# Kernel tuning notes

Measured on AMD Instinct MI355X. Metric: run time of the kernel, lower is better.

Reference implementation:

```python
import jax, jax.numpy as jnp
import numpy as np


def _lstm_layer(x, w_ih, w_hh, b_ih, b_hh):
    """Single LSTM layer, batch_first x: [B, T, D] -> [B, T, H]. Gate order i,f,g,o."""
    B, T, _ = x.shape
    H = w_hh.shape[1]
    # Precompute input-to-gates for all timesteps: [B, T, 4H]
    xg = jnp.einsum('btd,gd->btg', x, w_ih) + b_ih + b_hh

    def step(carry, xg_t):
        h, c = carry
        g = xg_t + h @ w_hh.T  # [B, 4H]
        i, f, gg, o = jnp.split(g, 4, axis=-1)
        i = jax.nn.sigmoid(i)
        f = jax.nn.sigmoid(f)
        gg = jnp.tanh(gg)
        o = jax.nn.sigmoid(o)
        c = f * c + i * gg
        h = o * jnp.tanh(c)
        return (h, c), h

    h0 = jnp.zeros((B, H), x.dtype)
    (_, _), hs = jax.lax.scan(step, (h0, h0), jnp.swapaxes(xg, 0, 1))
    return jnp.swapaxes(hs, 0, 1)  # [B, T, H]


def setup_inputs() -> dict:
    key = jax.random.key(0)
    ks = jax.random.split(key, 11)
    B, T, E, H = 128, 512, 256, 512
    s_e = 1.0 / np.sqrt(H)
    inp = {
        'x': jax.random.normal(ks[0], (B, T, E), jnp.float32),
        'w_ih0': jax.random.uniform(ks[1], (4 * H, E), jnp.float32, -s_e, s_e),
        'w_hh0': jax.random.uniform(ks[2], (4 * H, H), jnp.float32, -s_e, s_e),
        'b_ih0': jax.random.uniform(ks[3], (4 * H,), jnp.float32, -s_e, s_e),
        'b_hh0': jax.random.uniform(ks[4], (4 * H,), jnp.float32, -s_e, s_e),
        'w_ih1': jax.random.uniform(ks[5], (4 * H, H), jnp.float32, -s_e, s_e),
        'w_hh1': jax.random.uniform(ks[6], (4 * H, H), jnp.float32, -s_e, s_e),
        'b_ih1': jax.random.uniform(ks[7], (4 * H,), jnp.float32, -s_e, s_e),
        'b_hh1': jax.random.uniform(ks[8], (4 * H,), jnp.float32, -s_e, s_e),
        'w_fc': jax.random.uniform(ks[9], (1, H), jnp.float32, -s_e, s_e),
        'b_fc': jax.random.uniform(ks[10], (1,), jnp.float32, -s_e, s_e),
    }
    return inp


def reference(x, w_ih0, w_hh0, b_ih0, b_hh0, w_ih1, w_hh1, b_ih1, b_hh1, w_fc, b_fc):
    h1 = _lstm_layer(x, w_ih0, w_hh0, b_ih0, b_hh0)   # [B, T, H]
    h2 = _lstm_layer(h1, w_ih1, w_hh1, b_ih1, b_hh1)  # [B, T, H]
    last = h2[:, -1, :]                               # [B, H]
    out = last @ w_fc.T + b_fc                        # [B, 1]
    return jax.nn.sigmoid(out)
```

## Files before the change

kernel.cpp:

```cpp
#include <hip/hip_runtime.h>

using u16    = unsigned short;
using u64_t  = unsigned long long;
using short4v = __attribute__((ext_vector_type(4))) short;
using short8 = __attribute__((ext_vector_type(8))) short;
using f32x4  = __attribute__((ext_vector_type(4))) float;

#define T_STEPS 512
#define BATCH   128
#define HDIM    512
#define EDIM    256
#define NWG     256
#define WGS     256
#define HPITCH  65536

__device__ __forceinline__ u16 f2bf(float f) {
  unsigned u = __float_as_uint(f);
  u += 0x7FFFu + ((u >> 16) & 1u);
  return (u16)(u >> 16);
}
__device__ __forceinline__ float bf2f(u16 h) {
  return __uint_as_float(((unsigned)h) << 16);
}
__device__ __forceinline__ float sigm(float x) { return 1.0f / (1.0f + __expf(-x)); }
__device__ __forceinline__ float ftanh(float x) { return 1.0f - 2.0f / (__expf(2.0f * x) + 1.0f); }

__device__ __forceinline__ u64_t cl8(const u16* p) {
  return __hip_atomic_load((const u64_t*)p, __ATOMIC_RELAXED, __HIP_MEMORY_SCOPE_AGENT);
}
__device__ __forceinline__ void cstore2(u16* p, u16 v) {
  __hip_atomic_store(p, v, __ATOMIC_RELAXED, __HIP_MEMORY_SCOPE_AGENT);
}
__device__ __forceinline__ void cstore4(int* p, int v) {
  __hip_atomic_store(p, v, __ATOMIC_RELAXED, __HIP_MEMORY_SCOPE_AGENT);
}
__device__ __forceinline__ int ld4(const int* p) {
  return __hip_atomic_load(p, __ATOMIC_RELAXED, __HIP_MEMORY_SCOPE_AGENT);
}
__device__ __forceinline__ int addag(int* p, int v) {
  return __hip_atomic_fetch_add(p, v, __ATOMIC_RELAXED, __HIP_MEMORY_SCOPE_AGENT);
}
__device__ __forceinline__ short8 mk8(u64_t lo, u64_t hi) {
  short4v a = __builtin_bit_cast(short4v, lo);
  short4v b = __builtin_bit_cast(short4v, hi);
  return __builtin_shufflevector(a, b, 0, 1, 2, 3, 4, 5, 6, 7);
}

__global__ void cvt_bf16_kernel(const float* __restrict__ src, u16* __restrict__ dst, int n4) {
  int i = blockIdx.x * blockDim.x + threadIdx.x;
  if (i >= n4) return;
  float4 v = ((const float4*)src)[i];
  uint2 o;
  o.x = (unsigned)f2bf(v.x) | ((unsigned)f2bf(v.y) << 16);
  o.y = (unsigned)f2bf(v.z) | ((unsigned)f2bf(v.w) << 16);
  ((uint2*)dst)[i] = o;
}


__device__ __forceinline__ void grid_barrier(int* cnt, int* root, int* rel,
                                             int it, int tid, int bid) {
  __syncthreads();
  if (tid == 0) {
    int* mycnt = cnt + (bid >> 5) * 64;
    int old = addag(mycnt, 1);
    if (old == 32 * (it + 1) - 1) {
      int r = addag(root, 1);
      if (r == 8 * (it + 1) - 1) cstore4(rel, it + 1);
    }
    while (ld4(rel) < it + 1) __builtin_amdgcn_s_sleep(1);
  }
  __syncthreads();
}

__global__ void __launch_bounds__(WGS, 1) lstm_kernel(
    const float* __restrict__ wih0, const float* __restrict__ whh0,
    const float* __restrict__ bih0, const float* __restrict__ bhh0,
    const float* __restrict__ wih1, const float* __restrict__ whh1,
    const float* __restrict__ bih1, const float* __restrict__ bhh1,
    const float* __restrict__ wfc,  const float* __restrict__ bfc,
    const u16* __restrict__ xbf, u16* __restrict__ h0buf, u16* __restrict__ h1buf,
    float* __restrict__ out, int* syncp, int hist)
{
  extern __shared__ u16 smem[];
  u16* Ws_in  = smem;
  u16* Ws_rec = smem + 16384;

  const int tid    = threadIdx.x;
  const int bid    = blockIdx.x;
  const int layer  = bid >> 7;
  const int lb     = bid & 127;
  const int mhalf  = lb & 1;
  const int nc     = lb >> 1;
  const int jbase  = nc * 8;
  const int w      = tid >> 6;
  const int lane   = tid & 63;
  const int l15    = lane & 15;
  const int q      = lane >> 4;
  const int wmbase = mhalf * 64 + w * 16;
  const int gid    = layer * 2 + mhalf;

  char* sb = (char*)syncp;

  const int K_in = layer ? HDIM : EDIM;
  const float* Wih = layer ? wih1 : wih0;
  const float* Whh = layer ? whh1 : whh0;
  const float* Bih = layer ? bih1 : bih0;
  const float* Bhh = layer ? bhh1 : bhh0;

  for (int p = tid; p < 32 * (K_in / 8); p += WGS) {
    int c = p >> 5, n = p & 31;
    int grow = (n >> 3) * HDIM + jbase + (n & 7);
    const float* s = Wih + (size_t)grow * K_in + c * 8;
    u16* d = Ws_in + p * 8;
    #pragma unroll
    for (int e = 0; e < 8; ++e) d[e] = f2bf(s[e]);
  }
  for (int p = tid; p < 32 * (HDIM / 8); p += WGS) {
    int c = p >> 5, n = p & 31;
    int grow = (n >> 3) * HDIM + jbase + (n & 7);
    const float* s = Whh + (size_t)grow * HDIM + c * 8;
    u16* d = Ws_rec + p * 8;
    #pragma unroll
    for (int e = 0; e < 8; ++e) d[e] = f2bf(s[e]);
  }

  const int cc = l15 & 7;
  const float bi_i = Bih[0*HDIM + jbase + cc] + Bhh[0*HDIM + jbase + cc];
  const float bi_f = Bih[1*HDIM + jbase + cc] + Bhh[1*HDIM + jbase + cc];
  const float bi_g = Bih[2*HDIM + jbase + cc] + Bhh[2*HDIM + jbase + cc];
  const float bi_o = Bih[3*HDIM + jbase + cc] + Bhh[3*HDIM + jbase + cc];

  __syncthreads();

  float cst[4] = {0.f, 0.f, 0.f, 0.f};
  u16* ownbuf = layer ? h1buf : h0buf;
  const int arow = wmbase + l15;
  const size_t cbase = ((size_t)q * 128 + arow) * 8;

  auto MM2 = [&](short8 a, const u16* Ws, int kk, f32x4& A0, f32x4& A1) {
    const u16* bb = Ws + (kk * 4 + q) * 256 + l15 * 8;
    short8 b0 = *(const short8*)bb;
    short8 b1 = *(const short8*)(bb + 128);
    A0 = __builtin_amdgcn_mfma_f32_16x16x32_bf16(a, b0, A0, 0, 0, 0);
    A1 = __builtin_amdgcn_mfma_f32_16x16x32_bf16(a, b1, A1, 0, 0, 0);
  };

  if (hist) {
    int* my_stamp = (int*)(sb + 4096 + (size_t)gid * 256 + (size_t)nc * 4);
    const int* own_st = (const int*)(sb + 4096 + (size_t)gid * 256);
    const int* l0_st  = (const int*)(sb + 4096 + (size_t)mhalf * 256);

    for (int t = 0; t < T_STEPS; ++t) {
      short8 xfr[8];
      if (layer == 0) {
        const u16* xb = xbf + ((size_t)arow * T_STEPS + t) * EDIM + q * 8;
        #pragma unroll
        for (int kk = 0; kk < 8; ++kk) xfr[kk] = *(const short8*)(xb + kk * 32);
      }

      if (w == 0) {
        if (layer == 0) {
          if (t > 0) {
            for (;;) { int s = ld4(own_st + lane); if (__all(s >= t)) break; }
          }
        } else {
          for (;;) {
            int s  = ld4(own_st + lane);
            int s0 = ld4(l0_st + lane);
            if (__all((s >= t) && (s0 >= t + 1))) break;
          }
        }
      }
      __syncthreads();

      short8 ifr[16];
      short8 rfr[16];
      if (layer == 1) {
        const u16* ab = h0buf + (size_t)t * HPITCH + cbase;
        #pragma unroll
        for (int kk = 0; kk < 16; ++kk) ifr[kk] = *(const short8*)(ab + kk * 4096);
      }
      if (t > 0) {
        const u16* rb = ownbuf + (size_t)(t - 1) * HPITCH + cbase;
        #pragma unroll
        for (int kk = 0; kk < 16; ++kk) rfr[kk] = *(const short8*)(rb + kk * 4096);
      }

      f32x4 a0A = {0,0,0,0}, a1A = {0,0,0,0}, a0B = {0,0,0,0}, a1B = {0,0,0,0};
      if (layer == 0) {
        #pragma unroll
        for (int kk = 0; kk < 8; ++kk)
          MM2(xfr[kk], Ws_in, kk, (kk & 1) ? a0B : a0A, (kk & 1) ? a1B : a1A);
      } else {
        #pragma unroll
        for (int kk = 0; kk < 16; ++kk)
          MM2(ifr[kk], Ws_in, kk, (kk & 1) ? a0B : a0A, (kk & 1) ? a1B : a1A);
      }
      if (t > 0) {
        #pragma unroll
        for (int kk = 0; kk < 16; ++kk)
          MM2(rfr[kk], Ws_rec, kk, (kk & 1) ? a0B : a0A, (kk & 1) ? a1B : a1A);
      }
      f32x4 acc0 = a0A + a0B;
      f32x4 acc1 = a1A + a1B;

      u16* hw = ownbuf + (size_t)t * HPITCH + (size_t)nc * 1024;
      const bool low = (l15 < 8);
      #pragma unroll
      for (int r = 0; r < 4; ++r) {
        float a0 = acc0[r], a1 = acc1[r];
        float p0 = __shfl_xor(a0, 8);
        float p1 = __shfl_xor(a1, 8);
        float iv = low ? a0 : p0;
        float fv = low ? p0 : a0;
        float gv = low ? a1 : p1;
        float ov = low ? p1 : a1;
        iv = sigm(iv + bi_i);
        fv = sigm(fv + bi_f);
        gv = ftanh(gv + bi_g);
        ov = sigm(ov + bi_o);
        float cn = fv * cst[r] + iv * gv;
        cst[r] = cn;
        float hv = ov * ftanh(cn);
        if (low) cstore2(&hw[(size_t)(wmbase + q * 4 + r) * 8 + cc], f2bf(hv));
      }

      asm volatile("s_waitcnt vmcnt(0)" ::: "memory");
      __syncthreads();
      if (tid == 0) cstore4(my_stamp, t + 1);
    }

    if (bid == NWG - 1) {
      const int* g2 = (const int*)(sb + 4096 + (size_t)2 * 256);
      const int* g3 = (const int*)(sb + 4096 + (size_t)3 * 256);
      if (w == 0) {
        for (;;) {
          int a = ld4(g2 + lane);
          int b = ld4(g3 + lane);
          if (__all((a >= T_STEPS) && (b >= T_STEPS))) break;
        }
      }
      __syncthreads();
      __builtin_amdgcn_fence(__ATOMIC_ACQUIRE, "agent");
      const int b = tid >> 1, half = tid & 1;
      const u16* hp = h1buf + (size_t)(T_STEPS - 1) * HPITCH;
      const float* wf = wfc + half * 256;
      float s = 0.f;
      for (int cg = 0; cg < 32; ++cg) {
        const u16* p = hp + ((size_t)(half * 32 + cg) * 128 + b) * 8;
        #pragma unroll
        for (int e = 0; e < 8; ++e) s += bf2f(p[e]) * wf[cg * 8 + e];
      }
      s += __shfl_xor(s, 1);
      if (half == 0) out[b] = sigm(s + bfc[0]);
    }
    return;
  }

  int* f_cnt  = (int*)(sb + 8192);
  int* f_root = (int*)(sb + 10240);
  int* f_rel  = (int*)(sb + 10368);
  for (int it = 0; it <= T_STEPS; ++it) {
    const int t = layer ? (it - 1) : it;
    if (t >= 0 && t < T_STEPS) {
      short8 ifr[16];
      short8 rfr[16];
      short8 xfr[8];
      if (layer == 1) {
        const u16* ab = h0buf + (size_t)(t & 1) * HPITCH + cbase;
        #pragma unroll
        for (int kk = 0; kk < 16; ++kk)
          ifr[kk] = mk8(cl8(ab + kk * 4096), cl8(ab + kk * 4096 + 4));
      }
      if (t > 0) {
        const u16* rb = ownbuf + (size_t)((t - 1) & 1) * HPITCH + cbase;
        #pragma unroll
        for (int kk = 0; kk < 16; ++kk)
          rfr[kk] = mk8(cl8(rb + kk * 4096), cl8(rb + kk * 4096 + 4));
      }
      if (layer == 0) {
        const u16* xb = xbf + ((size_t)arow * T_STEPS + t) * EDIM + q * 8;
        #pragma unroll
        for (int kk = 0; kk < 8; ++kk) xfr[kk] = *(const short8*)(xb + kk * 32);
      }

      f32x4 a0A = {0,0,0,0}, a1A = {0,0,0,0}, a0B = {0,0,0,0}, a1B = {0,0,0,0};
      if (layer == 0) {
        #pragma unroll
        for (int kk = 0; kk < 8; ++kk)
          MM2(xfr[kk], Ws_in, kk, (kk & 1) ? a0B : a0A, (kk & 1) ? a1B : a1A);
      } else {
        #pragma unroll
        for (int kk = 0; kk < 16; ++kk)
          MM2(ifr[kk], Ws_in, kk, (kk & 1) ? a0B : a0A, (kk & 1) ? a1B : a1A);
      }
      if (t > 0) {
        #pragma unroll
        for (int kk = 0; kk < 16; ++kk)
          MM2(rfr[kk], Ws_rec, kk, (kk & 1) ? a0B : a0A, (kk & 1) ? a1B : a1A);
      }
      f32x4 acc0 = a0A + a0B;
      f32x4 acc1 = a1A + a1B;

      u16* hw = ownbuf + (size_t)(t & 1) * HPITCH + (size_t)nc * 1024;
      const bool low = (l15 < 8);
      #pragma unroll
      for (int r = 0; r < 4; ++r) {
        float a0 = acc0[r], a1 = acc1[r];
        float p0 = __shfl_xor(a0, 8);
        float p1 = __shfl_xor(a1, 8);
        float iv = low ? a0 : p0;
        float fv = low ? p0 : a0;
        float gv = low ? a1 : p1;
        float ov = low ? p1 : a1;
        iv = sigm(iv + bi_i);
        fv = sigm(fv + bi_f);
        gv = ftanh(gv + bi_g);
        ov = sigm(ov + bi_o);
        float cn = fv * cst[r] + iv * gv;
        cst[r] = cn;
        float hv = ov * ftanh(cn);
        if (low) cstore2(&hw[(size_t)(wmbase + q * 4 + r) * 8 + cc], f2bf(hv));
      }
    }
    grid_barrier(f_cnt, f_root, f_rel, it, tid, bid);
  }
  if (bid == NWG - 1) {
    __builtin_amdgcn_fence(__ATOMIC_ACQUIRE, "agent");
    const int b = tid >> 1, half = tid & 1;
    const u16* hp = h1buf + (size_t)1 * HPITCH;
    const float* wf = wfc + half * 256;
    float s = 0.f;
    for (int cg = 0; cg < 32; ++cg) {
      const u16* p = hp + ((size_t)(half * 32 + cg) * 128 + b) * 8;
      #pragma unroll
      for (int e = 0; e < 8; ++e) s += bf2f(p[e]) * wf[cg * 8 + e];
    }
    s += __shfl_xor(s, 1);
    if (half == 0) out[b] = sigm(s + bfc[0]);
  }
}

extern "C" void kernel_launch(void* const* d_in, const int* in_sizes, int n_in,
                              void* d_out, int out_size, void* d_ws, size_t ws_size,
                              hipStream_t stream) {
  (void)in_sizes; (void)n_in; (void)out_size;
  const float* x    = (const float*)d_in[0];
  const float* wih0 = (const float*)d_in[1];
  const float* whh0 = (const float*)d_in[2];
  const float* bih0 = (const float*)d_in[3];
  const float* bhh0 = (const float*)d_in[4];
  const float* wih1 = (const float*)d_in[5];
  const float* whh1 = (const float*)d_in[6];
  const float* bih1 = (const float*)d_in[7];
  const float* bhh1 = (const float*)d_in[8];
  const float* wfc  = (const float*)d_in[9];
  const float* bfc  = (const float*)d_in[10];
  float* outp = (float*)d_out;

  char* ws = (char*)d_ws;
  int*  syncp = (int*)ws;
  u16*  xbf   = (u16*)(ws + 32768);
  u16*  h0    = (u16*)(ws + 32768 + 33554432);

  const size_t need_hist = 32768ull + 33554432ull + 2ull * T_STEPS * HPITCH * sizeof(u16);
  const int hist = (ws_size >= need_hist) ? 1 : 0;
  const size_t slots = hist ? T_STEPS : 2;
  u16* h1 = h0 + slots * HPITCH;

  hipMemsetAsync(d_ws, 0, 32768, stream);

  const int n4 = (BATCH * T_STEPS * EDIM) / 4;
  cvt_bf16_kernel<<<n4 / 256, 256, 0, stream>>>(x, xbf, n4);

  hipFuncSetAttribute((const void*)lstm_kernel,
                      hipFuncAttributeMaxDynamicSharedMemorySize, 65536);

  void* args[] = { (void*)&wih0, (void*)&whh0, (void*)&bih0, (void*)&bhh0,
                   (void*)&wih1, (void*)&whh1, (void*)&bih1, (void*)&bhh1,
                   (void*)&wfc,  (void*)&bfc,
                   (void*)&xbf,  (void*)&h0,   (void*)&h1,
                   (void*)&outp, (void*)&syncp, (void*)&hist };
  hipLaunchCooperativeKernel((void*)lstm_kernel, dim3(NWG), dim3(WGS),
                             args, 65536, stream);
}
```

Measured before the change: 2.982 ms.

## Replace per-workgroup stamp polling with hierarchical atomic counters and replicated release flags

Workgroups now bump an atomic sub-counter per group of 8 instead of writing their own stamp. The last arriver in each group writes four replicated release flags, which spreads polling traffic over separate cache lines. Waiting is split so layer 0 computes its input projection before waiting on the recurrent dependency, and layer 1 waits only on the layer-0 release before its input matmul. The explicit vmcnt wait before the stamp write is dropped, leaving ordering to the atomic, which could risk visibility of h stores. The scratch layout offsets are moved to make room.

```diff
diff --git a/kernel.cpp b/kernel.cpp
--- a/kernel.cpp
+++ b/kernel.cpp
@@ -146,61 +146,60 @@
   };
 
   if (hist) {
-    int* my_stamp = (int*)(sb + 4096 + (size_t)gid * 256 + (size_t)nc * 4);
-    const int* own_st = (const int*)(sb + 4096 + (size_t)gid * 256);
-    const int* l0_st  = (const int*)(sb + 4096 + (size_t)mhalf * 256);
+    char* rel2 = sb + 12288;
+    int* sub_cnt = (int*)(sb + (size_t)gid * 2048 + (size_t)(nc >> 3) * 256);
+    const int myrep = nc & 3;
+    const int* pl_own = (const int*)(rel2 + (((size_t)gid * 8 + (lane & 7)) * 4 + myrep) * 128);
+    const int* pl_l0  = (const int*)(rel2 + (((size_t)mhalf * 8 + (lane & 7)) * 4 + myrep) * 128);
+    int* my_rel = (int*)(rel2 + ((size_t)gid * 8 + (nc >> 3)) * 4 * 128);
 
     for (int t = 0; t < T_STEPS; ++t) {
-      short8 xfr[8];
+      f32x4 a0A = {0,0,0,0}, a1A = {0,0,0,0}, a0B = {0,0,0,0}, a1B = {0,0,0,0};
+
       if (layer == 0) {
+        short8 xfr[8];
         const u16* xb = xbf + ((size_t)arow * T_STEPS + t) * EDIM + q * 8;
         #pragma unroll
         for (int kk = 0; kk < 8; ++kk) xfr[kk] = *(const short8*)(xb + kk * 32);
-      }
-
-      if (w == 0) {
-        if (layer == 0) {
-          if (t > 0) {
-            for (;;) { int s = ld4(own_st + lane); if (__all(s >= t)) break; }
-          }
-        } else {
-          for (;;) {
-            int s  = ld4(own_st + lane);
-            int s0 = ld4(l0_st + lane);
-            if (__all((s >= t) && (s0 >= t + 1))) break;
-          }
-        }
-      }
-      __syncthreads();
-
-      short8 ifr[16];
-      short8 rfr[16];
-      if (layer == 1) {
-        const u16* ab = h0buf + (size_t)t * HPITCH + cbase;
-        #pragma unroll
-        for (int kk = 0; kk < 16; ++kk) ifr[kk] = *(const short8*)(ab + kk * 4096);
-      }
-      if (t > 0) {
-        const u16* rb = ownbuf + (size_t)(t - 1) * HPITCH + cbase;
-        #pragma unroll
-        for (int kk = 0; kk < 16; ++kk) rfr[kk] = *(const short8*)(rb + kk * 4096);
-      }
-
-      f32x4 a0A = {0,0,0,0}, a1A = {0,0,0,0}, a0B = {0,0,0,0}, a1B = {0,0,0,0};
-      if (layer == 0) {
         #pragma unroll
         for (int kk = 0; kk < 8; ++kk)
           MM2(xfr[kk], Ws_in, kk, (kk & 1) ? a0B : a0A, (kk & 1) ? a1B : a1A);
       } else {
+        if (w == 0) {
+          for (;;) {
+            bool ok = true;
+            if (lane >= 8 && lane < 16) ok = (ld4(pl_l0) >= t + 1);
+            if (__all(ok)) break;
+          }
+        }
+        __syncthreads();
+        short8 ifr[16];
+        const u16* ab = h0buf + (size_t)t * HPITCH + cbase;
+        #pragma unroll
+        for (int kk = 0; kk < 16; ++kk) ifr[kk] = *(const short8*)(ab + kk * 4096);
         #pragma unroll
         for (int kk = 0; kk < 16; ++kk)
           MM2(ifr[kk], Ws_in, kk, (kk & 1) ? a0B : a0A, (kk & 1) ? a1B : a1A);
       }
+
       if (t > 0) {
+        if (w == 0) {
+          for (;;) {
+            bool ok = true;
+            if (lane < 8) ok = (ld4(pl_own) >= t);
+            if (__all(ok)) break;
+          }
+        }
+        __syncthreads();
+        short8 rfr[16];
+        const u16* rb = ownbuf + (size_t)(t - 1) * HPITCH + cbase;
+        #pragma unroll
+        for (int kk = 0; kk < 16; ++kk) rfr[kk] = *(const short8*)(rb + kk * 4096);
         #pragma unroll
         for (int kk = 0; kk < 16; ++kk)
           MM2(rfr[kk], Ws_rec, kk, (kk & 1) ? a0B : a0A, (kk & 1) ? a1B : a1A);
       }
+
       f32x4 acc0 = a0A + a0B;
       f32x4 acc1 = a1A + a1B;
 
@@ -225,19 +224,26 @@
         if (low) cstore2(&hw[(size_t)(wmbase + q * 4 + r) * 8 + cc], f2bf(hv));
       }
 
-      asm volatile("s_waitcnt vmcnt(0)" ::: "memory");
       __syncthreads();
-      if (tid == 0) cstore4(my_stamp, t + 1);
+      if (tid == 0) {
+        int old = addag(sub_cnt, 1);
+        if (old == 8 * (t + 1) - 1) {
+          #pragma unroll
+          for (int rp = 0; rp < 4; ++rp)
+            cstore4((int*)((char*)my_rel + (size_t)rp * 128), t + 1);
+        }
+      }
     }
 
     if (bid == NWG - 1) {
-      const int* g2 = (const int*)(sb + 4096 + (size_t)2 * 256);
-      const int* g3 = (const int*)(sb + 4096 + (size_t)3 * 256);
       if (w == 0) {
         for (;;) {
-          int a = ld4(g2 + lane);
-          int b = ld4(g3 + lane);
-          if (__all((a >= T_STEPS) && (b >= T_STEPS))) break;
+          bool ok = true;
+          if (lane < 8)
+            ok = (ld4((const int*)(rel2 + ((size_t)2 * 8 + lane) * 4 * 128)) >= T_STEPS);
+          else if (lane < 16)
+            ok = (ld4((const int*)(rel2 + ((size_t)3 * 8 + (lane - 8)) * 4 * 128)) >= T_STEPS);
+          if (__all(ok)) break;
         }
       }
       __syncthreads();
@@ -259,7 +265,7 @@
 
   int* f_cnt  = (int*)(sb + 8192);
   int* f_root = (int*)(sb + 10240);
-  int* f_rel  = (int*)(sb + 10368);
+  int* f_rel  = (int*)(sb + 10496);
   for (int it = 0; it <= T_STEPS; ++it) {
     const int t = layer ? (it - 1) : it;
     if (t >= 0 && t < T_STEPS) {
```

New measurement: 2.558 ms. 14.2% less time.
